# Optimization experiments

Measured on AMD Instinct MI355X. Metric: run time of the kernel, lower is better.

## Reference

```python
import jax, jax.numpy as jnp
import numpy as np

B, T, N = 8, 12, 256
T_IN = S_IN = P_IN = 32
O_IN = 64
HID = 64
OUT = 64
HEADS = 4


def setup_inputs() -> dict:
    key = jax.random.key(0)
    ks = jax.random.split(key, 26)
    f = lambda k, shape: jax.random.normal(k, shape, jnp.float32) * 0.05
    return {
        'x': jax.random.normal(ks[0], (B, T, N, O_IN), jnp.float32),
        'adj': jax.random.randint(ks[1], (B, T, N, N), 0, 2, jnp.int32),
        'te': jax.random.normal(ks[2], (B, T, T_IN), jnp.float32),
        'se': jax.random.normal(ks[3], (N, S_IN), jnp.float32),
        'pe': jax.random.normal(ks[4], (N, P_IN), jnp.float32),
        # SPGAT linear layers
        'Wt': f(ks[5], (T_IN, HID)), 'bt': f(ks[6], (HID,)),
        'Ws': f(ks[7], (S_IN, HID)), 'bs': f(ks[8], (HID,)),
        'Wp': f(ks[9], (P_IN, HID)), 'bp': f(ks[10], (HID,)),
        'Wfc': f(ks[11], (HID, OUT)), 'bfc': f(ks[12], (OUT,)),
        'Wout': f(ks[13], (2 * OUT, OUT)), 'bout': f(ks[14], (OUT,)),
        # GAT layer 1 (heads=HEADS, concat)
        'W1': f(ks[15], (O_IN, HEADS * HID)), 'b1': f(ks[16], (HEADS * HID,)),
        'a1_src': f(ks[17], (HEADS, HID)), 'a1_dst': f(ks[18], (HEADS, HID)),
        # GAT layer 2 (heads=1)
        'W2': f(ks[19], (HEADS * HID, OUT)), 'b2': f(ks[20], (OUT,)),
        'a2_src': f(ks[21], (1, OUT)), 'a2_dst': f(ks[22], (1, OUT)),
    }


def _gat_conv(h, mask, W, b, a_src, a_dst, heads):
    # h: [B,T,N,Fin]; mask: [B,T,N,N] bool, mask[...,i,j] => edge i->j (coo row=src, col=dst)
    d = W.shape[1] // heads
    hp = (h @ W).reshape(h.shape[0], h.shape[1], h.shape[2], heads, d)  # [B,T,N,H,d]
    es = jnp.einsum('btnhd,hd->bthn', hp, a_src)  # source attention logits
    ed = jnp.einsum('btnhd,hd->bthn', hp, a_dst)  # target attention logits
    # scores[...,h,i,j] = leaky(es_i + ed_j), softmax over sources i per target j
    sc = jax.nn.leaky_relu(es[..., :, None] + ed[..., None, :], 0.2)  # [B,T,H,N,N]
    sc = jnp.where(mask[:, :, None, :, :], sc, jnp.float32(-1e9))
    alpha = jax.nn.softmax(sc, axis=-2)
    out = jnp.einsum('bthij,btihd->btjhd', alpha, hp)  # aggregate at target j
    return out.reshape(h.shape[0], h.shape[1], h.shape[2], heads * d) + b


def reference(x, adj, te, se, pe, Wt, bt, Ws, bs, Wp, bp, Wfc, bfc, Wout, bout,
              W1, b1, a1_src, a1_dst, W2, b2, a2_src, a2_dst):
    mask = adj != 0
    t = (te @ Wt + bt) @ Wfc + bfc          # [B,T,OUT]
    s = (se @ Ws + bs) @ Wfc + bfc          # [N,OUT]
    p = (pe @ Wp + bp) @ Wfc + bfc          # [N,OUT]
    sp = jnp.concatenate([s, p], axis=-1) @ Wout + bout  # [N,OUT]
    st = sp[None, None, :, :] + t[:, :, None, :]         # [B,T,N,OUT]
    h = jax.nn.elu(_gat_conv(x, mask, W1, b1, a1_src, a1_dst, HEADS))
    od = _gat_conv(h, mask, W2, b2, a2_src, a2_dst, 1)   # [B,T,N,OUT]
    return jnp.concatenate([od, st], axis=-1) @ Wout + bout
```

## Files before the change

kernel.cpp:

```cpp
#include <hip/hip_runtime.h>
#include <hip/hip_bf16.h>
#include <cstdint>

#define NNODE 256
#define NBT   96
#define LOG2E 1.4426950408889634f

typedef __attribute__((ext_vector_type(8))) short short8;
typedef __attribute__((ext_vector_type(4))) float f32x4;

__device__ __forceinline__ unsigned pack_bf16x2(float a, float b) {
  unsigned ua = __float_as_uint(a);
  unsigned ub = __float_as_uint(b);
  unsigned ra = (ua + 0x7FFFu + ((ua >> 16) & 1u)) >> 16;
  unsigned rb = ((ub + 0x7FFFu + ((ub >> 16) & 1u)) >> 16) << 16;
  return ra | rb;
}
__device__ __forceinline__ unsigned short bf16_rn(float a) {
  unsigned ua = __float_as_uint(a);
  return (unsigned short)((ua + 0x7FFFu + ((ua >> 16) & 1u)) >> 16);
}

__global__ __launch_bounds__(256) void pack_mask_kernel(const int* __restrict__ adj,
                                                        unsigned* __restrict__ mb) {
  const int bt = blockIdx.x, w = blockIdx.y, j = threadIdx.x;
  const int* a = adj + (size_t)bt * NNODE * NNODE + (size_t)w * 32 * NNODE;
  unsigned v = 0;
#pragma unroll
  for (int b = 0; b < 32; ++b)
    v |= (a[b * NNODE + j] != 0 ? 1u : 0u) << b;
  mb[((size_t)bt * 8 + w) * 256 + j] = v;
}

__global__ __launch_bounds__(64) void embed_kernel(
    const float* __restrict__ te, const float* __restrict__ se, const float* __restrict__ pe,
    const float* __restrict__ Wt, const float* __restrict__ bt_,
    const float* __restrict__ Ws, const float* __restrict__ bs_,
    const float* __restrict__ Wp, const float* __restrict__ bp_,
    const float* __restrict__ Wfc, const float* __restrict__ bfc,
    const float* __restrict__ Wout, const float* __restrict__ bout,
    float* __restrict__ tW, float* __restrict__ spW) {
  const int j = threadIdx.x;
  __shared__ float A[64], Bv[64], C[64], D[64];
  const int blk = blockIdx.x;
  if (blk < NBT) {
    const int row = blk;
    float h = bt_[j];
    for (int k = 0; k < 32; ++k) h += te[row * 32 + k] * Wt[k * 64 + j];
    A[j] = h;
    __syncthreads();
    float tv = bfc[j];
    for (int k = 0; k < 64; ++k) tv += A[k] * Wfc[k * 64 + j];
    Bv[j] = tv;
    __syncthreads();
    float tw = bout[j];
    for (int d = 0; d < 64; ++d) tw += Bv[d] * Wout[(64 + d) * 64 + j];
    tW[row * 64 + j] = tw;
  } else {
    const int n = blk - NBT;
    float sh = bs_[j], ph = bp_[j];
    for (int k = 0; k < 32; ++k) {
      sh += se[n * 32 + k] * Ws[k * 64 + j];
      ph += pe[n * 32 + k] * Wp[k * 64 + j];
    }
    A[j] = sh; Bv[j] = ph;
    __syncthreads();
    float sv = bfc[j], pv = bfc[j];
    for (int k = 0; k < 64; ++k) {
      sv += A[k] * Wfc[k * 64 + j];
      pv += Bv[k] * Wfc[k * 64 + j];
    }
    C[j] = sv; D[j] = pv;
    __syncthreads();
    float spv = bout[j];
    for (int k = 0; k < 64; ++k)
      spv += C[k] * Wout[k * 64 + j] + D[k] * Wout[(64 + k) * 64 + j];
    __syncthreads();
    A[j] = spv;
    __syncthreads();
    float spw = 0.f;
    for (int d = 0; d < 64; ++d) spw += A[d] * Wout[(64 + d) * 64 + j];
    spW[n * 64 + j] = spw;
  }
}

__global__ __launch_bounds__(256) void prep_kernel(
    const float* __restrict__ Wout, const float* __restrict__ W1,
    const float* __restrict__ W2, unsigned short* __restrict__ WoT,
    unsigned short* __restrict__ W1T, unsigned short* __restrict__ W2T) {
  const int tid = threadIdx.x;
  if (blockIdx.x == 0) {
    {
      const int c = tid >> 2, d0 = (tid & 3) * 16;
#pragma unroll
      for (int i = 0; i < 16; ++i)
        WoT[c * 64 + d0 + i] = bf16_rn(Wout[(size_t)(d0 + i) * 64 + c]);
    }
    const int k = tid;
#pragma unroll
    for (int d = 0; d < 64; ++d)
      W2T[d * 256 + k] = bf16_rn(W2[(size_t)k * 64 + d]);
  } else {
    const int hd = tid;
    unsigned u[32];
#pragma unroll
    for (int p = 0; p < 32; ++p) {
      float a = W1[(size_t)(2 * p) * 256 + hd];
      float b = W1[(size_t)(2 * p + 1) * 256 + hd];
      u[p] = pack_bf16x2(a, b);
    }
    unsigned* o = (unsigned*)(W1T + (size_t)hd * 64);
#pragma unroll
    for (int p = 0; p < 8; ++p) {
      uint4 v;
      v.x = u[4 * p + 0]; v.y = u[4 * p + 1];
      v.z = u[4 * p + 2]; v.w = u[4 * p + 3];
      *reinterpret_cast<uint4*>(o + 4 * p) = v;
    }
  }
}

__global__ __launch_bounds__(512, 2) void fused1_kernel(
    const float* __restrict__ x, const unsigned* __restrict__ W1Tu,
    const unsigned* __restrict__ mbg, const float* __restrict__ a1s,
    const float* __restrict__ a1d, const float* __restrict__ b1,
    unsigned* __restrict__ hgl) {
  const int bt = blockIdx.x, head = blockIdx.y, z = blockIdx.z, tid = threadIdx.x;
  __shared__ union U {
    unsigned xb[256][36];
    unsigned hpT[64][132];
    unsigned short ob[128][72];
  } sm;
  __shared__ unsigned w1t[64][36];
  __shared__ unsigned mbs[1024];
  __shared__ float ess[256], eds[128], asv[64], adv[64];

  if (tid < 256) {
    const float* xrow = x + ((size_t)bt * NNODE + tid) * 64;
    unsigned u[32];
#pragma unroll
    for (int p = 0; p < 16; ++p) {
      float4 v = reinterpret_cast<const float4*>(xrow)[p];
      u[2 * p] = pack_bf16x2(v.x, v.y);
      u[2 * p + 1] = pack_bf16x2(v.z, v.w);
    }
#pragma unroll
    for (int p = 0; p < 8; ++p) {
      uint4 v; v.x = u[4 * p]; v.y = u[4 * p + 1]; v.z = u[4 * p + 2]; v.w = u[4 * p + 3];
      *reinterpret_cast<uint4*>(&sm.xb[tid][4 * p]) = v;
    }
    const int w = tid >> 5, col = (tid & 31) * 4;
    *reinterpret_cast<uint4*>(&mbs[w * 128 + col]) =
        *reinterpret_cast<const uint4*>(&mbg[(size_t)bt * 2048 + w * 256 + z * 128 + col]);
  } else {
    const int tt = tid - 256;
#pragma unroll
    for (int c = 0; c < 2; ++c) {
      const int idx = tt * 2 + c;
      const int r = idx >> 3, c4 = (idx & 7) * 4;
      *reinterpret_cast<uint4*>(&w1t[r][c4]) =
          *reinterpret_cast<const uint4*>(&W1Tu[(size_t)(head * 64 + r) * 32 + c4]);
    }
    if (tt < 64) asv[tt] = a1s[head * 64 + tt];
    else if (tt < 128) adv[tt - 64] = a1d[head * 64 + (tt - 64)];
  }
  __syncthreads();

  const int lane = tid & 63, wv = tid >> 6;
  const int m = lane & 15, q = lane >> 4;
  const f32x4 z4 = {0.f, 0.f, 0.f, 0.f};

  f32x4 cf[4][2];
#pragma unroll
  for (int mt = 0; mt < 4; ++mt)
#pragma unroll
    for (int nt = 0; nt < 2; ++nt) cf[mt][nt] = z4;
#pragma unroll
  for (int kt = 0; kt < 2; ++kt) {
    short8 af[4], bf[2];
#pragma unroll
    for (int mt = 0; mt < 4; ++mt)
      af[mt] = *reinterpret_cast<const short8*>(&w1t[mt * 16 + m][kt * 16 + q * 4]);
#pragma unroll
    for (int nt = 0; nt < 2; ++nt)
      bf[nt] = *reinterpret_cast<const short8*>(&sm.xb[wv * 32 + nt * 16 + m][kt * 16 + q * 4]);
#pragma unroll
    for (int mt = 0; mt < 4; ++mt)
#pragma unroll
      for (int nt = 0; nt < 2; ++nt)
        cf[mt][nt] = __builtin_amdgcn_mfma_f32_16x16x32_bf16(af[mt], bf[nt], cf[mt][nt], 0, 0, 0);
  }
  __syncthreads();

  {
    unsigned short* hpT16 = reinterpret_cast<unsigned short*>(&sm.hpT[0][0]);
#pragma unroll
    for (int mt = 0; mt < 4; ++mt)
#pragma unroll
      for (int nt = 0; nt < 2; ++nt)
#pragma unroll
        for (int reg = 0; reg < 4; ++reg) {
          const int d = mt * 16 + q * 4 + reg;
          const int n = wv * 32 + nt * 16 + m;
          hpT16[d * 264 + n] = bf16_rn(cf[mt][nt][reg]);
        }
  }
  __syncthreads();

  if (tid < 256) {
    const int n = tid;
    const unsigned sh = (n & 1) * 16;
    float s = 0.f;
#pragma unroll 8
    for (int d = 0; d < 64; ++d) {
      unsigned u = sm.hpT[d][n >> 1];
      s += __uint_as_float((u >> sh) << 16) * asv[d];
    }
    ess[n] = s * LOG2E;
  } else if (tid < 384) {
    const int jl = tid - 256;
    const int n = z * 128 + jl;
    const unsigned sh = (n & 1) * 16;
    float s = 0.f;
#pragma unroll 8
    for (int d = 0; d < 64; ++d) {
      unsigned u = sm.hpT[d][n >> 1];
      s += __uint_as_float((u >> sh) << 16) * adv[d];
    }
    eds[jl] = s * LOG2E;
  }
  __syncthreads();

  f32x4 cacc[4], cden = z4;
#pragma unroll
  for (int nt = 0; nt < 4; ++nt) cacc[nt] = z4;
  const float edv = eds[wv * 16 + m];
  const short8 ones8 = {(short)0x3F80, (short)0x3F80, (short)0x3F80, (short)0x3F80,
                        (short)0x3F80, (short)0x3F80, (short)0x3F80, (short)0x3F80};

  for (int kt = 0; kt < 8; ++kt) {
    short8 bfr[4];
#pragma unroll
    for (int nt = 0; nt < 4; ++nt)
      bfr[nt] = *reinterpret_cast<const short8*>(&sm.hpT[nt * 16 + m][kt * 16 + q * 4]);
    float e[8];
    *reinterpret_cast<float4*>(&e[0]) = *reinterpret_cast<const float4*>(&ess[kt * 32 + q * 8]);
    *reinterpret_cast<float4*>(&e[4]) = *reinterpret_cast<const float4*>(&ess[kt * 32 + q * 8 + 4]);
    const unsigned bits = mbs[kt * 128 + wv * 16 + m] >> (q * 8);
    float pv[8];
#pragma unroll
    for (int r = 0; r < 8; ++r) {
      float sc = e[r] + edv;
      sc = fmaxf(sc, 0.2f * sc);
      pv[r] = ((bits >> r) & 1u) ? exp2f(sc) : 0.f;
    }
    union { unsigned u[4]; short8 s; } A;
#pragma unroll
    for (int h = 0; h < 4; ++h) A.u[h] = pack_bf16x2(pv[2 * h], pv[2 * h + 1]);
#pragma unroll
    for (int nt = 0; nt < 4; ++nt)
      cacc[nt] = __builtin_amdgcn_mfma_f32_16x16x32_bf16(A.s, bfr[nt], cacc[nt], 0, 0, 0);
    cden = __builtin_amdgcn_mfma_f32_16x16x32_bf16(A.s, ones8, cden, 0, 0, 0);
  }
  __syncthreads();

  float b1v[4];
#pragma unroll
  for (int nt = 0; nt < 4; ++nt) b1v[nt] = b1[head * 64 + nt * 16 + m];
#pragma unroll
  for (int reg = 0; reg < 4; ++reg) {
    const int jl = wv * 16 + q * 4 + reg;
    const float inv = 1.f / fmaxf(cden[reg], 1e-30f);
#pragma unroll
    for (int nt = 0; nt < 4; ++nt) {
      float v = cacc[nt][reg] * inv + b1v[nt];
      v = v > 0.f ? v : expm1f(v);
      sm.ob[jl][nt * 16 + m] = bf16_rn(v);
    }
  }
  __syncthreads();

  unsigned* go = hgl + (size_t)bt * 32768 + (size_t)z * 128 * 128 + head * 32;
#pragma unroll
  for (int c = 0; c < 2; ++c) {
    const int idx = tid * 2 + c;
    const int jl = idx >> 3, c4 = (idx & 7) * 4;
    *reinterpret_cast<uint4*>(&go[(size_t)jl * 128 + c4]) =
        *reinterpret_cast<const uint4*>(&sm.ob[jl][c4 * 2]);
  }
}

__global__ __launch_bounds__(256, 2) void feat2_kernel(
    const unsigned* __restrict__ hglu, const unsigned* __restrict__ W2Tu,
    unsigned short* __restrict__ hpT2) {
  const int bt = blockIdx.x, ng = blockIdx.y, tid = threadIdx.x;
  __shared__ unsigned hb[64][132];
  __shared__ unsigned w2t[64][132];

#pragma unroll
  for (int c = 0; c < 8; ++c) {
    int i4 = tid + c * 256;
    int row = i4 >> 5, col = (i4 & 31) << 2;
    *reinterpret_cast<uint4*>(&hb[row][col]) =
        *reinterpret_cast<const uint4*>(&hglu[((size_t)bt * 256 + ng * 64 + row) * 128 + col]);
    *reinterpret_cast<uint4*>(&w2t[row][col]) =
        *reinterpret_cast<const uint4*>(&W2Tu[row * 128 + col]);
  }
  __syncthreads();

  const int lane = tid & 63, wv = tid >> 6;
  const int m = lane & 15, q = lane >> 4;
  const f32x4 z4 = {0.f, 0.f, 0.f, 0.f};
  f32x4 cf[4];
#pragma unroll
  for (int mt = 0; mt < 4; ++mt) cf[mt] = z4;

  for (int kt = 0; kt < 8; ++kt) {
    short8 bf = *reinterpret_cast<const short8*>(&hb[wv * 16 + m][kt * 16 + q * 4]);
#pragma unroll
    for (int mt = 0; mt < 4; ++mt) {
      short8 af = *reinterpret_cast<const short8*>(&w2t[mt * 16 + m][kt * 16 + q * 4]);
      cf[mt] = __builtin_amdgcn_mfma_f32_16x16x32_bf16(af, bf, cf[mt], 0, 0, 0);
    }
  }

  unsigned short* go = hpT2 + (size_t)bt * 16384;
#pragma unroll
  for (int mt = 0; mt < 4; ++mt)
#pragma unroll
    for (int reg = 0; reg < 4; ++reg) {
      const int d = mt * 16 + q * 4 + reg;
      const int n = ng * 64 + wv * 16 + m;
      go[d * 256 + n] = bf16_rn(cf[mt][reg]);
    }
}

__global__ __launch_bounds__(512, 2) void agg2_kernel(
    const unsigned* __restrict__ hpT2u, const unsigned* __restrict__ mbg,
    const float* __restrict__ a2s, const float* __restrict__ a2d,
    const float* __restrict__ b2, const unsigned* __restrict__ WoTu,
    const float* __restrict__ spW, const float* __restrict__ tW,
    float* __restrict__ out) {
  const int bt = blockIdx.x, jh = blockIdx.y, tid = threadIdx.x;
  const int jbase = jh * 128;
  __shared__ union U2 {
    unsigned hpT[64][132];
    unsigned short ob[128][72];
  } sm;
  __shared__ unsigned wol[64][36];
  __shared__ unsigned mbs[8 * 128];
  __shared__ float ess[256], eds[128];
  __shared__ float a2sv[64], a2dv[64];

  const unsigned* gh = hpT2u + (size_t)bt * 8192;
#pragma unroll
  for (int c = 0; c < 4; ++c) {
    int i4 = tid + c * 512;
    int row = i4 >> 5, col = (i4 & 31) << 2;
    *reinterpret_cast<uint4*>(&sm.hpT[row][col]) =
        *reinterpret_cast<const uint4*>(&gh[row * 128 + col]);
  }
  {
    int row = tid >> 3, col = (tid & 7) * 4;
    *reinterpret_cast<uint4*>(&wol[row][col]) =
        *reinterpret_cast<const uint4*>(&WoTu[row * 32 + col]);
  }
  if (tid < 256) {
    int w = tid >> 5, col = (tid & 31) * 4;
    *reinterpret_cast<uint4*>(&mbs[w * 128 + col]) =
        *reinterpret_cast<const uint4*>(&mbg[(size_t)bt * 2048 + w * 256 + jbase + col]);
  }
  if (tid >= 384 && tid < 448) a2sv[tid - 384] = a2s[tid - 384];
  else if (tid >= 448) a2dv[tid - 448] = a2d[tid - 448];
  __syncthreads();

  if (tid < 256) {
    const int n = tid;
    const unsigned sh = (n & 1) * 16;
    float s = 0.f;
#pragma unroll 8
    for (int d = 0; d < 64; ++d) {
      unsigned u = sm.hpT[d][n >> 1];
      s += __uint_as_float((u >> sh) << 16) * a2sv[d];
    }
    ess[n] = s * LOG2E;
  } else if (tid < 384) {
    const int jl = tid - 256;
    const int n = jbase + jl;
    const unsigned sh = (n & 1) * 16;
    float s = 0.f;
#pragma unroll 8
    for (int d = 0; d < 64; ++d) {
      unsigned u = sm.hpT[d][n >> 1];
      s += __uint_as_float((u >> sh) << 16) * a2dv[d];
    }
    eds[jl] = s * LOG2E;
  }
  __syncthreads();

  const int lane = tid & 63, wv = tid >> 6;
  const int m = lane & 15, q = lane >> 4;
  const f32x4 z4 = {0.f, 0.f, 0.f, 0.f};
  f32x4 cacc[4], cden = z4;
#pragma unroll
  for (int nt = 0; nt < 4; ++nt) cacc[nt] = z4;
  const float edv = eds[wv * 16 + m];
  const short8 ones8 = {(short)0x3F80, (short)0x3F80, (short)0x3F80, (short)0x3F80,
                        (short)0x3F80, (short)0x3F80, (short)0x3F80, (short)0x3F80};

  for (int kt = 0; kt < 8; ++kt) {
    short8 bfr[4];
#pragma unroll
    for (int nt = 0; nt < 4; ++nt)
      bfr[nt] = *reinterpret_cast<const short8*>(&sm.hpT[nt * 16 + m][kt * 16 + q * 4]);
    float e[8];
    *reinterpret_cast<float4*>(&e[0]) = *reinterpret_cast<const float4*>(&ess[kt * 32 + q * 8]);
    *reinterpret_cast<float4*>(&e[4]) = *reinterpret_cast<const float4*>(&ess[kt * 32 + q * 8 + 4]);
    const unsigned bits = mbs[kt * 128 + wv * 16 + m] >> (q * 8);
    float pv[8];
#pragma unroll
    for (int r = 0; r < 8; ++r) {
      float sc = e[r] + edv;
      sc = fmaxf(sc, 0.2f * sc);
      pv[r] = ((bits >> r) & 1u) ? exp2f(sc) : 0.f;
    }
    union { unsigned u[4]; short8 s; } A;
#pragma unroll
    for (int h = 0; h < 4; ++h) A.u[h] = pack_bf16x2(pv[2 * h], pv[2 * h + 1]);
#pragma unroll
    for (int nt = 0; nt < 4; ++nt)
      cacc[nt] = __builtin_amdgcn_mfma_f32_16x16x32_bf16(A.s, bfr[nt], cacc[nt], 0, 0, 0);
    cden = __builtin_amdgcn_mfma_f32_16x16x32_bf16(A.s, ones8, cden, 0, 0, 0);
  }
  __syncthreads();

  float b2v[4];
#pragma unroll
  for (int nt = 0; nt < 4; ++nt) b2v[nt] = b2[nt * 16 + m];
#pragma unroll
  for (int reg = 0; reg < 4; ++reg) {
    const int jl = wv * 16 + q * 4 + reg;
    const float inv = 1.f / fmaxf(cden[reg], 1e-30f);
#pragma unroll
    for (int nt = 0; nt < 4; ++nt)
      sm.ob[jl][nt * 16 + m] = bf16_rn(cacc[nt][reg] * inv + b2v[nt]);
  }
  __syncthreads();

  f32x4 c2[4];
#pragma unroll
  for (int ct = 0; ct < 4; ++ct) c2[ct] = z4;
#pragma unroll
  for (int kt2 = 0; kt2 < 2; ++kt2) {
    short8 a2f = *reinterpret_cast<const short8*>(&sm.ob[wv * 16 + m][kt2 * 32 + q * 8]);
#pragma unroll
    for (int ct = 0; ct < 4; ++ct) {
      short8 bw = *reinterpret_cast<const short8*>(&wol[ct * 16 + m][kt2 * 16 + q * 4]);
      c2[ct] = __builtin_amdgcn_mfma_f32_16x16x32_bf16(a2f, bw, c2[ct], 0, 0, 0);
    }
  }
  float tWv[4];
#pragma unroll
  for (int ct = 0; ct < 4; ++ct) tWv[ct] = tW[bt * 64 + ct * 16 + m];
#pragma unroll
  for (int reg = 0; reg < 4; ++reg) {
    const int j = jbase + wv * 16 + q * 4 + reg;
#pragma unroll
    for (int ct = 0; ct < 4; ++ct) {
      const int cc = ct * 16 + m;
      out[((size_t)bt * NNODE + j) * 64 + cc] =
          c2[ct][reg] + spW[j * 64 + cc] + tWv[ct];
    }
  }
}

extern "C" void kernel_launch(void* const* d_in, const int* in_sizes, int n_in,
                              void* d_out, int out_size, void* d_ws, size_t ws_size,
                              hipStream_t stream) {
  const float* x    = (const float*)d_in[0];
  const int*   adj  = (const int*)d_in[1];
  const float* te   = (const float*)d_in[2];
  const float* se   = (const float*)d_in[3];
  const float* pe   = (const float*)d_in[4];
  const float* Wt   = (const float*)d_in[5];
  const float* bt_  = (const float*)d_in[6];
  const float* Ws   = (const float*)d_in[7];
  const float* bs_  = (const float*)d_in[8];
  const float* Wp   = (const float*)d_in[9];
  const float* bp_  = (const float*)d_in[10];
  const float* Wfc  = (const float*)d_in[11];
  const float* bfc  = (const float*)d_in[12];
  const float* Wout = (const float*)d_in[13];
  const float* bout = (const float*)d_in[14];
  const float* W1   = (const float*)d_in[15];
  const float* b1   = (const float*)d_in[16];
  const float* a1s  = (const float*)d_in[17];
  const float* a1d  = (const float*)d_in[18];
  const float* W2   = (const float*)d_in[19];
  const float* b2   = (const float*)d_in[20];
  const float* a2s  = (const float*)d_in[21];
  const float* a2d  = (const float*)d_in[22];

  char* ws = (char*)d_ws;
  unsigned*       mb   = (unsigned*)(ws);
  float*          tW   = (float*)(ws + 786432);
  float*          spW  = (float*)(ws + 811008);
  unsigned short* WoT  = (unsigned short*)(ws + 876544);
  unsigned short* W1T  = (unsigned short*)(ws + 884736);
  unsigned short* W2T  = (unsigned short*)(ws + 917504);
  unsigned short* hpT  = (unsigned short*)(ws + 950272);
  unsigned*       hgl  = (unsigned*)(ws + 13533184);

  pack_mask_kernel<<<dim3(NBT, 8), 256, 0, stream>>>(adj, mb);
  embed_kernel<<<NBT + NNODE, 64, 0, stream>>>(te, se, pe, Wt, bt_, Ws, bs_,
                                               Wp, bp_, Wfc, bfc, Wout, bout, tW, spW);
  prep_kernel<<<2, 256, 0, stream>>>(Wout, W1, W2, WoT, W1T, W2T);
  fused1_kernel<<<dim3(NBT, 4, 2), 512, 0, stream>>>(x, (const unsigned*)W1T, mb,
                                                     a1s, a1d, b1, hgl);
  feat2_kernel<<<dim3(NBT, 4), 256, 0, stream>>>(hgl, (const unsigned*)W2T, hpT);
  agg2_kernel<<<dim3(NBT, 2), 512, 0, stream>>>((const unsigned*)hpT, mb, a2s, a2d,
                                                b2, (const unsigned*)WoT, spW, tW,
                                                (float*)d_out);
}
```

Measured before the change: 168.6 us.

## Merge setup kernels into one launch and fuse layer-2 feature GEMM into aggregation

Combines mask packing, embedding precompute and weight transposes into a single setup kernel with a block-index dispatch, cutting two launches. Also folds the layer-2 feature projection (h @ W2) into the aggregation kernel, computing hp for all 256 nodes in shared memory per block, so the hpT2 global round trip and one launch go away. The cost is that each of the two j-halves recomputes the full projection, doubling that GEMM work, and the setup blocks that use only 64 of 256 threads waste lanes.

```diff
diff --git a/kernel.cpp b/kernel.cpp
--- a/kernel.cpp
+++ b/kernel.cpp
@@ -21,75 +21,83 @@
   return (unsigned short)((ua + 0x7FFFu + ((ua >> 16) & 1u)) >> 16);
 }
 
-__global__ __launch_bounds__(256) void pack_mask_kernel(const int* __restrict__ adj,
-                                                        unsigned* __restrict__ mb) {
-  const int bt = blockIdx.x, w = blockIdx.y, j = threadIdx.x;
-  const int* a = adj + (size_t)bt * NNODE * NNODE + (size_t)w * 32 * NNODE;
-  unsigned v = 0;
-#pragma unroll
-  for (int b = 0; b < 32; ++b)
-    v |= (a[b * NNODE + j] != 0 ? 1u : 0u) << b;
-  mb[((size_t)bt * 8 + w) * 256 + j] = v;
-}
-
-__global__ __launch_bounds__(64) void embed_kernel(
+__global__ __launch_bounds__(256) void setup_kernel(
+    const int* __restrict__ adj, unsigned* __restrict__ mb,
     const float* __restrict__ te, const float* __restrict__ se, const float* __restrict__ pe,
     const float* __restrict__ Wt, const float* __restrict__ bt_,
     const float* __restrict__ Ws, const float* __restrict__ bs_,
     const float* __restrict__ Wp, const float* __restrict__ bp_,
     const float* __restrict__ Wfc, const float* __restrict__ bfc,
     const float* __restrict__ Wout, const float* __restrict__ bout,
-    float* __restrict__ tW, float* __restrict__ spW) {
-  const int j = threadIdx.x;
+    const float* __restrict__ W1, const float* __restrict__ W2,
+    float* __restrict__ tW, float* __restrict__ spW,
+    unsigned short* __restrict__ WoT, unsigned short* __restrict__ W1T,
+    unsigned short* __restrict__ W2T) {
+  const int blk = blockIdx.x, tid = threadIdx.x;
   __shared__ float A[64], Bv[64], C[64], D[64];
-  const int blk = blockIdx.x;
-  if (blk < NBT) {
-    const int row = blk;
-    float h = bt_[j];
-    for (int k = 0; k < 32; ++k) h += te[row * 32 + k] * Wt[k * 64 + j];
-    A[j] = h;
-    __syncthreads();
-    float tv = bfc[j];
-    for (int k = 0; k < 64; ++k) tv += A[k] * Wfc[k * 64 + j];
-    Bv[j] = tv;
-    __syncthreads();
-    float tw = bout[j];
-    for (int d = 0; d < 64; ++d) tw += Bv[d] * Wout[(64 + d) * 64 + j];
-    tW[row * 64 + j] = tw;
-  } else {
-    const int n = blk - NBT;
-    float sh = bs_[j], ph = bp_[j];
-    for (int k = 0; k < 32; ++k) {
-      sh += se[n * 32 + k] * Ws[k * 64 + j];
-      ph += pe[n * 32 + k] * Wp[k * 64 + j];
-    }
-    A[j] = sh; Bv[j] = ph;
-    __syncthreads();
-    float sv = bfc[j], pv = bfc[j];
-    for (int k = 0; k < 64; ++k) {
-      sv += A[k] * Wfc[k * 64 + j];
-      pv += Bv[k] * Wfc[k * 64 + j];
-    }
-    C[j] = sv; D[j] = pv;
-    __syncthreads();
-    float spv = bout[j];
-    for (int k = 0; k < 64; ++k)
-      spv += C[k] * Wout[k * 64 + j] + D[k] * Wout[(64 + k) * 64 + j];
-    __syncthreads();
-    A[j] = spv;
-    __syncthreads();
-    float spw = 0.f;
-    for (int d = 0; d < 64; ++d) spw += A[d] * Wout[(64 + d) * 64 + j];
-    spW[n * 64 + j] = spw;
-  }
-}
-
-__global__ __launch_bounds__(256) void prep_kernel(
-    const float* __restrict__ Wout, const float* __restrict__ W1,
-    const float* __restrict__ W2, unsigned short* __restrict__ WoT,
-    unsigned short* __restrict__ W1T, unsigned short* __restrict__ W2T) {
-  const int tid = threadIdx.x;
-  if (blockIdx.x == 0) {
+
+  if (blk < 768) {
+    const int bt = blk >> 3, w = blk & 7, j = tid;
+    const int* a = adj + (size_t)bt * NNODE * NNODE + (size_t)w * 32 * NNODE;
+    unsigned v = 0;
+#pragma unroll
+    for (int b = 0; b < 32; ++b)
+      v |= (a[b * NNODE + j] != 0 ? 1u : 0u) << b;
+    mb[((size_t)bt * 8 + w) * 256 + j] = v;
+  } else if (blk < 864) {
+    const int row = blk - 768, j = tid & 63;
+    if (tid < 64) {
+      float h = bt_[j];
+      for (int k = 0; k < 32; ++k) h += te[row * 32 + k] * Wt[k * 64 + j];
+      A[j] = h;
+    }
+    __syncthreads();
+    if (tid < 64) {
+      float tv = bfc[j];
+      for (int k = 0; k < 64; ++k) tv += A[k] * Wfc[k * 64 + j];
+      Bv[j] = tv;
+    }
+    __syncthreads();
+    if (tid < 64) {
+      float tw = bout[j];
+      for (int d = 0; d < 64; ++d) tw += Bv[d] * Wout[(64 + d) * 64 + j];
+      tW[row * 64 + j] = tw;
+    }
+  } else if (blk < 1120) {
+    const int n = blk - 864, j = tid & 63;
+    float spv = 0.f;
+    if (tid < 64) {
+      float sh = bs_[j], ph = bp_[j];
+      for (int k = 0; k < 32; ++k) {
+        sh += se[n * 32 + k] * Ws[k * 64 + j];
+        ph += pe[n * 32 + k] * Wp[k * 64 + j];
+      }
+      A[j] = sh; Bv[j] = ph;
+    }
+    __syncthreads();
+    if (tid < 64) {
+      float sv = bfc[j], pv = bfc[j];
+      for (int k = 0; k < 64; ++k) {
+        sv += A[k] * Wfc[k * 64 + j];
+        pv += Bv[k] * Wfc[k * 64 + j];
+      }
+      C[j] = sv; D[j] = pv;
+    }
+    __syncthreads();
+    if (tid < 64) {
+      spv = bout[j];
+      for (int k = 0; k < 64; ++k)
+        spv += C[k] * Wout[k * 64 + j] + D[k] * Wout[(64 + k) * 64 + j];
+    }
+    __syncthreads();
+    if (tid < 64) A[j] = spv;
+    __syncthreads();
+    if (tid < 64) {
+      float spw = 0.f;
+      for (int d = 0; d < 64; ++d) spw += A[d] * Wout[(64 + d) * 64 + j];
+      spW[n * 64 + j] = spw;
+    }
+  } else if (blk == 1120) {
     {
       const int c = tid >> 2, d0 = (tid & 3) * 16;
 #pragma unroll
@@ -290,76 +298,24 @@
   }
 }
 
-__global__ __launch_bounds__(256, 2) void feat2_kernel(
+__global__ __launch_bounds__(512, 2) void fused2_kernel(
     const unsigned* __restrict__ hglu, const unsigned* __restrict__ W2Tu,
-    unsigned short* __restrict__ hpT2) {
-  const int bt = blockIdx.x, ng = blockIdx.y, tid = threadIdx.x;
-  __shared__ unsigned hb[64][132];
-  __shared__ unsigned w2t[64][132];
-
-#pragma unroll
-  for (int c = 0; c < 8; ++c) {
-    int i4 = tid + c * 256;
-    int row = i4 >> 5, col = (i4 & 31) << 2;
-    *reinterpret_cast<uint4*>(&hb[row][col]) =
-        *reinterpret_cast<const uint4*>(&hglu[((size_t)bt * 256 + ng * 64 + row) * 128 + col]);
-    *reinterpret_cast<uint4*>(&w2t[row][col]) =
-        *reinterpret_cast<const uint4*>(&W2Tu[row * 128 + col]);
-  }
-  __syncthreads();
-
-  const int lane = tid & 63, wv = tid >> 6;
-  const int m = lane & 15, q = lane >> 4;
-  const f32x4 z4 = {0.f, 0.f, 0.f, 0.f};
-  f32x4 cf[4];
-#pragma unroll
-  for (int mt = 0; mt < 4; ++mt) cf[mt] = z4;
-
-  for (int kt = 0; kt < 8; ++kt) {
-    short8 bf = *reinterpret_cast<const short8*>(&hb[wv * 16 + m][kt * 16 + q * 4]);
-#pragma unroll
-    for (int mt = 0; mt < 4; ++mt) {
-      short8 af = *reinterpret_cast<const short8*>(&w2t[mt * 16 + m][kt * 16 + q * 4]);
-      cf[mt] = __builtin_amdgcn_mfma_f32_16x16x32_bf16(af, bf, cf[mt], 0, 0, 0);
-    }
-  }
-
-  unsigned short* go = hpT2 + (size_t)bt * 16384;
-#pragma unroll
-  for (int mt = 0; mt < 4; ++mt)
-#pragma unroll
-    for (int reg = 0; reg < 4; ++reg) {
-      const int d = mt * 16 + q * 4 + reg;
-      const int n = ng * 64 + wv * 16 + m;
-      go[d * 256 + n] = bf16_rn(cf[mt][reg]);
-    }
-}
-
-__global__ __launch_bounds__(512, 2) void agg2_kernel(
-    const unsigned* __restrict__ hpT2u, const unsigned* __restrict__ mbg,
-    const float* __restrict__ a2s, const float* __restrict__ a2d,
-    const float* __restrict__ b2, const unsigned* __restrict__ WoTu,
-    const float* __restrict__ spW, const float* __restrict__ tW,
-    float* __restrict__ out) {
+    const unsigned* __restrict__ mbg, const float* __restrict__ a2s,
+    const float* __restrict__ a2d, const float* __restrict__ b2,
+    const unsigned* __restrict__ WoTu, const float* __restrict__ spW,
+    const float* __restrict__ tW, float* __restrict__ out) {
   const int bt = blockIdx.x, jh = blockIdx.y, tid = threadIdx.x;
   const int jbase = jh * 128;
-  __shared__ union U2 {
+  __shared__ union U {
+    struct { unsigned h_c[256][36]; unsigned w2t_c[64][36]; } fs;
     unsigned hpT[64][132];
     unsigned short ob[128][72];
   } sm;
   __shared__ unsigned wol[64][36];
-  __shared__ unsigned mbs[8 * 128];
+  __shared__ unsigned mbs[1024];
   __shared__ float ess[256], eds[128];
   __shared__ float a2sv[64], a2dv[64];
 
-  const unsigned* gh = hpT2u + (size_t)bt * 8192;
-#pragma unroll
-  for (int c = 0; c < 4; ++c) {
-    int i4 = tid + c * 512;
-    int row = i4 >> 5, col = (i4 & 31) << 2;
-    *reinterpret_cast<uint4*>(&sm.hpT[row][col]) =
-        *reinterpret_cast<const uint4*>(&gh[row * 128 + col]);
-  }
   {
     int row = tid >> 3, col = (tid & 7) * 4;
     *reinterpret_cast<uint4*>(&wol[row][col]) =
@@ -372,6 +328,63 @@
   }
   if (tid >= 384 && tid < 448) a2sv[tid - 384] = a2s[tid - 384];
   else if (tid >= 448) a2dv[tid - 448] = a2d[tid - 448];
+
+  const int lane = tid & 63, wv = tid >> 6;
+  const int m = lane & 15, q = lane >> 4;
+  const f32x4 z4 = {0.f, 0.f, 0.f, 0.f};
+
+  f32x4 cf[4][2];
+#pragma unroll
+  for (int mt = 0; mt < 4; ++mt)
+#pragma unroll
+    for (int nt = 0; nt < 2; ++nt) cf[mt][nt] = z4;
+
+  for (int kc = 0; kc < 4; ++kc) {
+    __syncthreads();
+#pragma unroll
+    for (int c = 0; c < 4; ++c) {
+      int i4 = tid + c * 512;
+      int n = i4 >> 3, col = (i4 & 7) * 4;
+      *reinterpret_cast<uint4*>(&sm.fs.h_c[n][col]) =
+          *reinterpret_cast<const uint4*>(&hglu[(size_t)bt * 32768 + n * 128 + kc * 32 + col]);
+    }
+    {
+      int d = tid >> 3, col = (tid & 7) * 4;
+      *reinterpret_cast<uint4*>(&sm.fs.w2t_c[d][col]) =
+          *reinterpret_cast<const uint4*>(&W2Tu[d * 128 + kc * 32 + col]);
+    }
+    __syncthreads();
+#pragma unroll
+    for (int kt2 = 0; kt2 < 2; ++kt2) {
+      short8 af[4], bf[2];
+#pragma unroll
+      for (int mt = 0; mt < 4; ++mt)
+        af[mt] = *reinterpret_cast<const short8*>(&sm.fs.w2t_c[mt * 16 + m][kt2 * 16 + q * 4]);
+#pragma unroll
+      for (int nt = 0; nt < 2; ++nt)
+        bf[nt] = *reinterpret_cast<const short8*>(&sm.fs.h_c[wv * 32 + nt * 16 + m][kt2 * 16 + q * 4]);
+#pragma unroll
+      for (int mt = 0; mt < 4; ++mt)
+#pragma unroll
+        for (int nt = 0; nt < 2; ++nt)
+          cf[mt][nt] = __builtin_amdgcn_mfma_f32_16x16x32_bf16(af[mt], bf[nt], cf[mt][nt], 0, 0, 0);
+    }
+  }
+  __syncthreads();
+
+  {
+    unsigned short* hpT16 = reinterpret_cast<unsigned short*>(&sm.hpT[0][0]);
+#pragma unroll
+    for (int mt = 0; mt < 4; ++mt)
+#pragma unroll
+      for (int nt = 0; nt < 2; ++nt)
+#pragma unroll
+        for (int reg = 0; reg < 4; ++reg) {
+          const int d = mt * 16 + q * 4 + reg;
+          const int n = wv * 32 + nt * 16 + m;
+          hpT16[d * 264 + n] = bf16_rn(cf[mt][nt][reg]);
+        }
+  }
   __syncthreads();
 
   if (tid < 256) {
@@ -398,9 +411,6 @@
   }
   __syncthreads();
 
-  const int lane = tid & 63, wv = tid >> 6;
-  const int m = lane & 15, q = lane >> 4;
-  const f32x4 z4 = {0.f, 0.f, 0.f, 0.f};
   f32x4 cacc[4], cden = z4;
 #pragma unroll
   for (int nt = 0; nt < 4; ++nt) cacc[nt] = z4;
@@ -508,17 +518,14 @@
   unsigned short* WoT  = (unsigned short*)(ws + 876544);
   unsigned short* W1T  = (unsigned short*)(ws + 884736);
   unsigned short* W2T  = (unsigned short*)(ws + 917504);
-  unsigned short* hpT  = (unsigned short*)(ws + 950272);
   unsigned*       hgl  = (unsigned*)(ws + 13533184);
 
-  pack_mask_kernel<<<dim3(NBT, 8), 256, 0, stream>>>(adj, mb);
-  embed_kernel<<<NBT + NNODE, 64, 0, stream>>>(te, se, pe, Wt, bt_, Ws, bs_,
-                                               Wp, bp_, Wfc, bfc, Wout, bout, tW, spW);
-  prep_kernel<<<2, 256, 0, stream>>>(Wout, W1, W2, WoT, W1T, W2T);
+  setup_kernel<<<1122, 256, 0, stream>>>(adj, mb, te, se, pe, Wt, bt_, Ws, bs_,
+                                         Wp, bp_, Wfc, bfc, Wout, bout, W1, W2,
+                                         tW, spW, WoT, W1T, W2T);
   fused1_kernel<<<dim3(NBT, 4, 2), 512, 0, stream>>>(x, (const unsigned*)W1T, mb,
                                                      a1s, a1d, b1, hgl);
-  feat2_kernel<<<dim3(NBT, 4), 256, 0, stream>>>(hgl, (const unsigned*)W2T, hpT);
-  agg2_kernel<<<dim3(NBT, 2), 512, 0, stream>>>((const unsigned*)hpT, mb, a2s, a2d,
-                                                b2, (const unsigned*)WoT, spW, tW,
-                                                (float*)d_out);
+  fused2_kernel<<<dim3(NBT, 2), 512, 0, stream>>>(hgl, (const unsigned*)W2T, mb,
+                                                  a2s, a2d, b2, (const unsigned*)WoT,
+                                                  spW, tW, (float*)d_out);
 }
```

Result: no change. 169.8 us (+0.7%).
